# Kernel optimization log

Measured on AMD Instinct MI355X. Metric: run time of the kernel, lower is better.

Reference implementation:

```python
import jax, jax.numpy as jnp
import numpy as np

B, S, D = 256, 70, 128
NUM_NODE = 40000
N_SAMPLE = 12
ALPHA = 0.2  # leaky-relu slope


def setup_inputs() -> dict:
    key = jax.random.key(0)
    ks = jax.random.split(key, 16)
    stdv = 1.0 / np.sqrt(D)
    u = lambda k, shp: jax.random.uniform(k, shp, jnp.float32, -stdv, stdv)
    inputs = jax.random.randint(ks[0], (B, S), 0, NUM_NODE)
    adj = jax.random.randint(ks[1], (B, S, S), 0, 5)
    mask_item = jnp.ones((B, S), jnp.int32)
    item = jax.random.randint(ks[2], (B, S), 0, NUM_NODE)
    input_times = jax.random.uniform(ks[3], (B, S), jnp.float32)
    adj_all = jax.random.randint(ks[4], (NUM_NODE, N_SAMPLE), 0, NUM_NODE)
    num_w = jax.random.uniform(ks[5], (NUM_NODE, N_SAMPLE), jnp.float32)
    embedding = u(ks[6], (NUM_NODE, D))
    a0, a1, a2, a3 = (u(ks[7 + i], (D,)) for i in range(4))
    gw1 = u(ks[11], (D + 1, D))
    gw2 = u(ks[12], (D, 1))
    gw3 = u(ks[13], (2 * D, D))
    gbias = u(ks[14], (D,))
    return dict(inputs=inputs, adj=adj, mask_item=mask_item, item=item,
                input_times=input_times, adj_all=adj_all, num_w=num_w,
                embedding=embedding, a0=a0, a1=a1, a2=a2, a3=a3,
                gw1=gw1, gw2=gw2, gw3=gw3, gbias=gbias)


def reference(inputs, adj, mask_item, item, input_times, adj_all, num_w,
              embedding, a0, a1, a2, a3, gw1, gw2, gw3, gbias):
    # ---- local aggregator (4-relation GAT over session graph) ----
    h = embedding[inputs]                              # [B,S,D]
    a_in = h[:, :, None, :] * h[:, None, :, :]         # [B,S,S,D] pairwise products
    att = lambda a: jax.nn.leaky_relu(jnp.einsum('bijd,d->bij', a_in, a), ALPHA)
    e0, e1, e2, e3 = att(a0), att(a1), att(a2), att(a3)
    neg = jnp.full_like(e0, -9e15)
    alpha = jnp.where(adj == 1, e0, neg)
    alpha = jnp.where(adj == 2, e1, alpha)
    alpha = jnp.where(adj == 3, e2, alpha)
    alpha = jnp.where(adj == 4, e3, alpha)
    alpha = jax.nn.softmax(alpha, axis=-1)
    h_local = jnp.einsum('bij,bjd->bid', alpha, h)     # [B,S,D]

    # ---- global aggregator: 1-hop neighbor sampling + session-gated attention ----
    flat = inputs.reshape(-1)
    neigh = adj_all[flat].reshape(B, S, N_SAMPLE)      # sampled neighbor ids
    nw = num_w[flat].reshape(B, S, N_SAMPLE)           # neighbor co-occurrence weights
    nv = embedding[neigh]                              # [B,S,K,D]

    maskf = mask_item.astype(jnp.float32)[..., None]   # [B,S,1]
    item_emb = embedding[item] * maskf
    sess = jnp.sum(item_emb, axis=1) / jnp.sum(maskf, axis=1)   # [B,D] mean session emb
    extra = sess[:, None, None, :]                     # broadcast to [B,S,K,D]

    feat = jnp.concatenate([extra * nv, nw[..., None]], axis=-1)  # [B,S,K,D+1]
    al = jax.nn.leaky_relu(feat @ gw1, 0.2)            # [B,S,K,D]
    al = jax.nn.softmax((al @ gw2)[..., 0], axis=-1)[..., None]   # [B,S,K,1]
    nagg = jnp.sum(al * nv, axis=-2)                   # [B,S,D]

    out = jnp.concatenate([h, nagg], axis=-1) @ gw3 + gbias
    h_global = jax.nn.relu(out)                        # [B,S,D]
    # dropout_local/global = 0 (eval mode): identity
    return h_local, h_global
```

## Files before the change

kernel.cpp:

```cpp
#include <hip/hip_runtime.h>
#include <hip/hip_bf16.h>

#define B_ 256
#define S_ 70
#define D_ 128
#define NSAMP 12
#define HGLOB (B_ * S_ * D_)
#define IBLK 14
#define HTS 136
#define NPOS 10
#define NR2 (NPOS * NSAMP)
#define NRP 128

typedef float  f32x4 __attribute__((ext_vector_type(4)));
typedef short  s16x8 __attribute__((ext_vector_type(8)));

__device__ __forceinline__ unsigned short f2bf(float x) {
    union { float f; unsigned u; } v; v.f = x;
    return (unsigned short)((v.u + 0x7FFF + ((v.u >> 16) & 1)) >> 16);
}
__device__ __forceinline__ float bf2f(unsigned short u) {
    union { unsigned u; float f; } v; v.u = ((unsigned)u) << 16;
    return v.f;
}

__global__ __launch_bounds__(128) void sess_kernel(const int* __restrict__ item,
                                                   const int* __restrict__ mask,
                                                   const float* __restrict__ emb,
                                                   float* __restrict__ sess) {
    int b = blockIdx.x;
    int d = threadIdx.x;
    float acc = 0.f, msum = 0.f;
    for (int s = 0; s < S_; ++s) {
        int node = item[b * S_ + s];
        float m = (float)mask[b * S_ + s];
        acc += m * emb[(long)node * D_ + d];
        msum += m;
    }
    sess[b * D_ + d] = acc / msum;
}

__global__ __launch_bounds__(256) void pack_weights(const float* __restrict__ gw1,
                                                    const float* __restrict__ gw3,
                                                    unsigned short* __restrict__ gw1T,
                                                    unsigned short* __restrict__ gw3T) {
    int idx = blockIdx.x * 256 + threadIdx.x;
    if (idx < 128 * 128) {
        int c = idx >> 7, r = idx & 127;
        gw1T[idx] = f2bf(gw1[r * 128 + c]);
    }
    if (idx < 128 * 256) {
        int c = idx >> 8, r = idx & 255;
        gw3T[idx] = f2bf(gw3[r * 128 + c]);
    }
}

__global__ __launch_bounds__(256) void local_kernel(const int* __restrict__ inputs,
                                                    const int* __restrict__ adj,
                                                    const float* __restrict__ emb,
                                                    const float* __restrict__ a0p,
                                                    const float* __restrict__ a1p,
                                                    const float* __restrict__ a2p,
                                                    const float* __restrict__ a3p,
                                                    float* __restrict__ out) {
    __shared__ __align__(16) unsigned short hl[72 * 128];
    __shared__ __align__(16) unsigned short HT[128 * HTS];
    __shared__ __align__(16) float          El[16 * 84];
    __shared__ __align__(16) unsigned short al[16 * 104];
    __shared__ int ids[S_];

    const int b  = blockIdx.x;
    const int i0 = blockIdx.y * IBLK;
    const int tid  = threadIdx.x;
    const int lane = tid & 63, wave = tid >> 6;
    const int l15  = lane & 15, l4 = lane >> 4;

    const s16x8 zero8 = {0, 0, 0, 0, 0, 0, 0, 0};

    if (tid < S_) ids[tid] = inputs[b * S_ + tid];
    for (int c = tid; c < (128 * HTS) / 8; c += 256) ((s16x8*)HT)[c] = zero8;
    if (tid < 32) ((s16x8*)hl)[70 * 16 + tid] = zero8;
    __syncthreads();

    #pragma unroll
    for (int it = 0; it < 5; ++it) {
        int idx = it * 256 + tid;
        if (idx < S_ * 16) {
            int s = idx >> 4, c8 = idx & 15;
            const float4* ev = (const float4*)(emb + (long)ids[s] * D_ + c8 * 8);
            float4 e0 = ev[0], e1 = ev[1];
            s16x8 p;
            p[0] = (short)f2bf(e0.x); p[1] = (short)f2bf(e0.y);
            p[2] = (short)f2bf(e0.z); p[3] = (short)f2bf(e0.w);
            p[4] = (short)f2bf(e1.x); p[5] = (short)f2bf(e1.y);
            p[6] = (short)f2bf(e1.z); p[7] = (short)f2bf(e1.w);
            ((s16x8*)hl)[s * 16 + (c8 ^ (s & 7))] = p;
            #pragma unroll
            for (int e = 0; e < 8; ++e) {
                int d = c8 * 8 + e;
                HT[d * HTS + s] = (unsigned short)p[e];
            }
        }
    }
    __syncthreads();

    s16x8 af_all[4][4];
    {
        const float* aptr[4] = {a0p, a1p, a2p, a3p};
        int hrow = i0 + l15;
        #pragma unroll
        for (int ks = 0; ks < 4; ++ks) {
            s16x8 hf = ((s16x8*)hl)[hrow * 16 + ((ks * 4 + l4) ^ (hrow & 7))];
            #pragma unroll
            for (int r = 0; r < 4; ++r) {
                const float* ar = aptr[r];
                float4 alo = *(const float4*)(ar + ks * 32 + l4 * 8);
                float4 ahi = *(const float4*)(ar + ks * 32 + l4 * 8 + 4);
                s16x8 o;
                o[0] = (short)f2bf(bf2f((unsigned short)hf[0]) * alo.x);
                o[1] = (short)f2bf(bf2f((unsigned short)hf[1]) * alo.y);
                o[2] = (short)f2bf(bf2f((unsigned short)hf[2]) * alo.z);
                o[3] = (short)f2bf(bf2f((unsigned short)hf[3]) * alo.w);
                o[4] = (short)f2bf(bf2f((unsigned short)hf[4]) * ahi.x);
                o[5] = (short)f2bf(bf2f((unsigned short)hf[5]) * ahi.y);
                o[6] = (short)f2bf(bf2f((unsigned short)hf[6]) * ahi.z);
                o[7] = (short)f2bf(bf2f((unsigned short)hf[7]) * ahi.w);
                af_all[r][ks] = o;
            }
        }
    }

    for (int n = wave; n < 5; n += 4) {
        s16x8 bfr[4];
        int jr = n * 16 + l15;
        int jrc = jr < 72 ? jr : 71;
        #pragma unroll
        for (int ks = 0; ks < 4; ++ks)
            bfr[ks] = ((s16x8*)hl)[jrc * 16 + ((ks * 4 + l4) ^ (jrc & 7))];

        f32x4 ac0 = {0.f,0.f,0.f,0.f}, ac1 = {0.f,0.f,0.f,0.f};
        f32x4 ac2 = {0.f,0.f,0.f,0.f}, ac3 = {0.f,0.f,0.f,0.f};
        #pragma unroll
        for (int ks = 0; ks < 4; ++ks) {
            ac0 = __builtin_amdgcn_mfma_f32_16x16x32_bf16(af_all[0][ks], bfr[ks], ac0, 0, 0, 0);
            ac1 = __builtin_amdgcn_mfma_f32_16x16x32_bf16(af_all[1][ks], bfr[ks], ac1, 0, 0, 0);
            ac2 = __builtin_amdgcn_mfma_f32_16x16x32_bf16(af_all[2][ks], bfr[ks], ac2, 0, 0, 0);
            ac3 = __builtin_amdgcn_mfma_f32_16x16x32_bf16(af_all[3][ks], bfr[ks], ac3, 0, 0, 0);
        }

        #pragma unroll
        for (int reg = 0; reg < 4; ++reg) {
            int il = l4 * 4 + reg;
            int i  = i0 + il;
            int j  = n * 16 + l15;
            float v;
            if (j < S_) {
                int ic = i < S_ ? i : S_ - 1;
                int a  = adj[((long)b * S_ + ic) * S_ + j];
                float raw = (a == 1) ? ac0[reg] : (a == 2) ? ac1[reg]
                          : (a == 3) ? ac2[reg] : (a == 4) ? ac3[reg] : 0.f;
                v = (a >= 1 && a <= 4) ? (raw > 0.f ? raw : 0.2f * raw) : -9e15f;
            } else {
                v = -INFINITY;
            }
            El[il * 84 + j] = v;
        }
    }
    __syncthreads();

    {
        int g = tid >> 4, li = tid & 15;
        float mx = -INFINITY;
        for (int j = li; j < S_; j += 16) mx = fmaxf(mx, El[g * 84 + j]);
        #pragma unroll
        for (int o = 1; o < 16; o <<= 1) mx = fmaxf(mx, __shfl_xor(mx, o));
        float sm = 0.f;
        for (int j = li; j < S_; j += 16) {
            float ex = __expf(El[g * 84 + j] - mx);
            El[g * 84 + j] = ex;
            sm += ex;
        }
        #pragma unroll
        for (int o = 1; o < 16; o <<= 1) sm += __shfl_xor(sm, o);
        float inv = 1.f / sm;
        for (int j = li; j < 104; j += 16)
            al[g * 104 + j] = (j < S_) ? f2bf(El[g * 84 + j] * inv) : (unsigned short)0;
    }
    __syncthreads();

    for (int n = wave; n < 8; n += 4) {
        f32x4 acc = {0.f, 0.f, 0.f, 0.f};
        int d = n * 16 + l15;
        #pragma unroll
        for (int ks = 0; ks < 3; ++ks) {
            s16x8 afp = *(const s16x8*)(al + l15 * 104 + ks * 32 + l4 * 8);
            s16x8 bfp = *(const s16x8*)(HT + d * HTS + ks * 32 + l4 * 8);
            acc = __builtin_amdgcn_mfma_f32_16x16x32_bf16(afp, bfp, acc, 0, 0, 0);
        }
        #pragma unroll
        for (int reg = 0; reg < 4; ++reg) {
            int il = l4 * 4 + reg;
            if (il < IBLK)
                out[((long)b * S_ + (i0 + il)) * D_ + d] = acc[reg];
        }
    }
}

__global__ __launch_bounds__(256, 3) void global_kernel(
        const int* __restrict__ inputs, const int* __restrict__ adj_all,
        const float* __restrict__ num_w, const float* __restrict__ emb,
        const float* __restrict__ sess,
        const unsigned short* __restrict__ gw1T, const float* __restrict__ gw1,
        const float* __restrict__ gw2,
        const unsigned short* __restrict__ gw3T, const float* __restrict__ gbias,
        float* __restrict__ out) {
    __shared__ __align__(16) unsigned short nv[NRP * 128];
    __shared__ __align__(16) unsigned short cat[16 * 256];
    __shared__ int   neigh[NR2];
    __shared__ float nw[NR2];
    __shared__ float spart[NRP][4];
    __shared__ float score[NR2];
    __shared__ float wsm[NR2];

    const int tid  = threadIdx.x;
    const int lane = tid & 63, wave = tid >> 6;
    const int l15  = lane & 15, l4 = lane >> 4;
    const int b    = blockIdx.x;
    const int i0   = blockIdx.y * NPOS;
    const int bs0  = b * S_ + i0;

    const s16x8 zero8 = {0, 0, 0, 0, 0, 0, 0, 0};

    if (tid < NR2) {
        int p = tid / NSAMP;
        int k = tid - p * NSAMP;
        int node = inputs[bs0 + p];
        neigh[tid] = adj_all[node * NSAMP + k];
        nw[tid]    = num_w[node * NSAMP + k];
    }
    if (tid < 128) ((s16x8*)nv)[NR2 * 16 + tid] = zero8;
    __syncthreads();

    #pragma unroll
    for (int it = 0; it < 8; ++it) {
        int idx = it * 256 + tid;
        if (idx < NR2 * 16) {
            int row = idx >> 4, c8 = idx & 15;
            const float4* ev = (const float4*)(emb + (long)neigh[row] * D_ + c8 * 8);
            float4 e0 = ev[0], e1 = ev[1];
            s16x8 p;
            p[0] = (short)f2bf(e0.x); p[1] = (short)f2bf(e0.y);
            p[2] = (short)f2bf(e0.z); p[3] = (short)f2bf(e0.w);
            p[4] = (short)f2bf(e1.x); p[5] = (short)f2bf(e1.y);
            p[6] = (short)f2bf(e1.z); p[7] = (short)f2bf(e1.w);
            ((s16x8*)nv)[row * 16 + (c8 ^ (row & 7))] = p;
        }
    }
    __syncthreads();

    s16x8 bfp[2][4];
    #pragma unroll
    for (int n = 0; n < 2; ++n) {
        int c = (wave * 2 + n) * 16 + l15;
        #pragma unroll
        for (int ks = 0; ks < 4; ++ks) {
            s16x8 g = *(const s16x8*)(gw1T + c * 128 + ks * 32 + l4 * 8);
            float4 slo = *(const float4*)(sess + b * D_ + ks * 32 + l4 * 8);
            float4 shi = *(const float4*)(sess + b * D_ + ks * 32 + l4 * 8 + 4);
            s16x8 o;
            o[0] = (short)f2bf(bf2f((unsigned short)g[0]) * slo.x);
            o[1] = (short)f2bf(bf2f((unsigned short)g[1]) * slo.y);
            o[2] = (short)f2bf(bf2f((unsigned short)g[2]) * slo.z);
            o[3] = (short)f2bf(bf2f((unsigned short)g[3]) * slo.w);
            o[4] = (short)f2bf(bf2f((unsigned short)g[4]) * shi.x);
            o[5] = (short)f2bf(bf2f((unsigned short)g[5]) * shi.y);
            o[6] = (short)f2bf(bf2f((unsigned short)g[6]) * shi.z);
            o[7] = (short)f2bf(bf2f((unsigned short)g[7]) * shi.w);
            bfp[n][ks] = o;
        }
    }
    float g128a = gw1[128 * 128 + wave * 32 + l15];
    float g128b = gw1[128 * 128 + wave * 32 + 16 + l15];
    float gw2a  = gw2[wave * 32 + l15];
    float gw2b  = gw2[wave * 32 + 16 + l15];

    for (int m = 0; m < NRP / 16; ++m) {
        int arow = m * 16 + l15;
        s16x8 af[4];
        #pragma unroll
        for (int ks = 0; ks < 4; ++ks)
            af[ks] = ((s16x8*)nv)[arow * 16 + ((ks * 4 + l4) ^ (arow & 7))];

        f32x4 acc0 = {0.f, 0.f, 0.f, 0.f}, acc1 = {0.f, 0.f, 0.f, 0.f};
        #pragma unroll
        for (int ks = 0; ks < 4; ++ks) {
            acc0 = __builtin_amdgcn_mfma_f32_16x16x32_bf16(af[ks], bfp[0][ks], acc0, 0, 0, 0);
            acc1 = __builtin_amdgcn_mfma_f32_16x16x32_bf16(af[ks], bfp[1][ks], acc1, 0, 0, 0);
        }

        float sp[4];
        #pragma unroll
        for (int reg = 0; reg < 4; ++reg) {
            int r = m * 16 + l4 * 4 + reg;
            float nwv = (r < NR2) ? nw[r] : 0.f;
            float al0 = acc0[reg] + nwv * g128a;
            float al1 = acc1[reg] + nwv * g128b;
            al0 = al0 > 0.f ? al0 : 0.2f * al0;
            al1 = al1 > 0.f ? al1 : 0.2f * al1;
            sp[reg] = al0 * gw2a + al1 * gw2b;
        }
        #pragma unroll
        for (int off = 1; off < 16; off <<= 1) {
            #pragma unroll
            for (int reg = 0; reg < 4; ++reg) sp[reg] += __shfl_xor(sp[reg], off);
        }
        if (l15 == 0) {
            int rb = m * 16 + l4 * 4;
            #pragma unroll
            for (int reg = 0; reg < 4; ++reg) spart[rb + reg][wave] = sp[reg];
        }
    }
    __syncthreads();

    if (tid < NR2)
        score[tid] = spart[tid][0] + spart[tid][1] + spart[tid][2] + spart[tid][3];
    __syncthreads();

    if (tid < NPOS) {
        float mx = -1e30f;
        #pragma unroll
        for (int k = 0; k < NSAMP; ++k) mx = fmaxf(mx, score[tid * NSAMP + k]);
        float ex[NSAMP]; float ss = 0.f;
        #pragma unroll
        for (int k = 0; k < NSAMP; ++k) { ex[k] = __expf(score[tid * NSAMP + k] - mx); ss += ex[k]; }
        float inv = 1.f / ss;
        #pragma unroll
        for (int k = 0; k < NSAMP; ++k) wsm[tid * NSAMP + k] = ex[k] * inv;
    }
    __syncthreads();

    {
        int p  = tid >> 4;
        int c8 = tid & 15;
        if (p < NPOS) {
            float a0v[4] = {0.f,0.f,0.f,0.f}, a1v[4] = {0.f,0.f,0.f,0.f};
            #pragma unroll
            for (int k = 0; k < NSAMP; ++k) {
                int row = p * NSAMP + k;
                float w = wsm[row];
                s16x8 nvv = ((s16x8*)nv)[row * 16 + (c8 ^ (row & 7))];
                a0v[0] += w * bf2f((unsigned short)nvv[0]);
                a0v[1] += w * bf2f((unsigned short)nvv[1]);
                a0v[2] += w * bf2f((unsigned short)nvv[2]);
                a0v[3] += w * bf2f((unsigned short)nvv[3]);
                a1v[0] += w * bf2f((unsigned short)nvv[4]);
                a1v[1] += w * bf2f((unsigned short)nvv[5]);
                a1v[2] += w * bf2f((unsigned short)nvv[6]);
                a1v[3] += w * bf2f((unsigned short)nvv[7]);
            }
            int node = inputs[bs0 + p];
            const float4* hv = (const float4*)(emb + (long)node * D_ + c8 * 8);
            float4 h0 = hv[0], h1 = hv[1];
            s16x8 ph, pa;
            ph[0]=(short)f2bf(h0.x); ph[1]=(short)f2bf(h0.y); ph[2]=(short)f2bf(h0.z); ph[3]=(short)f2bf(h0.w);
            ph[4]=(short)f2bf(h1.x); ph[5]=(short)f2bf(h1.y); ph[6]=(short)f2bf(h1.z); ph[7]=(short)f2bf(h1.w);
            pa[0]=(short)f2bf(a0v[0]); pa[1]=(short)f2bf(a0v[1]); pa[2]=(short)f2bf(a0v[2]); pa[3]=(short)f2bf(a0v[3]);
            pa[4]=(short)f2bf(a1v[0]); pa[5]=(short)f2bf(a1v[1]); pa[6]=(short)f2bf(a1v[2]); pa[7]=(short)f2bf(a1v[3]);
            ((s16x8*)cat)[p * 32 + ( c8       ^ (p & 7))] = ph;
            ((s16x8*)cat)[p * 32 + ((16 + c8) ^ (p & 7))] = pa;
        } else {
            ((s16x8*)cat)[p * 32 + ( c8       ^ (p & 7))] = zero8;
            ((s16x8*)cat)[p * 32 + ((16 + c8) ^ (p & 7))] = zero8;
        }
    }
    __syncthreads();

    {
        f32x4 acc0 = {0.f,0.f,0.f,0.f}, acc1 = {0.f,0.f,0.f,0.f};
        int arow = l15;
        int cc = wave * 32 + l15;
        #pragma unroll
        for (int ks = 0; ks < 8; ++ks) {
            s16x8 a  = ((s16x8*)cat)[arow * 32 + ((ks * 4 + l4) ^ (arow & 7))];
            s16x8 b0 = *(const s16x8*)(gw3T +  cc       * 256 + ks * 32 + l4 * 8);
            s16x8 b1 = *(const s16x8*)(gw3T + (cc + 16) * 256 + ks * 32 + l4 * 8);
            acc0 = __builtin_amdgcn_mfma_f32_16x16x32_bf16(a, b0, acc0, 0, 0, 0);
            acc1 = __builtin_amdgcn_mfma_f32_16x16x32_bf16(a, b1, acc1, 0, 0, 0);
        }
        float gb0 = gbias[wave * 32 + l15];
        float gb1 = gbias[wave * 32 + 16 + l15];
        #pragma unroll
        for (int reg = 0; reg < 4; ++reg) {
            int il = l4 * 4 + reg;
            if (il < NPOS) {
                long bs = bs0 + il;
                float o0 = acc0[reg] + gb0;
                float o1 = acc1[reg] + gb1;
                out[(long)HGLOB + bs * D_ + wave * 32 + l15]      = o0 > 0.f ? o0 : 0.f;
                out[(long)HGLOB + bs * D_ + wave * 32 + 16 + l15] = o1 > 0.f ? o1 : 0.f;
            }
        }
    }
}

extern "C" void kernel_launch(void* const* d_in, const int* in_sizes, int n_in,
                              void* d_out, int out_size, void* d_ws, size_t ws_size,
                              hipStream_t stream) {
    const int*   inputs  = (const int*)  d_in[0];
    const int*   adj     = (const int*)  d_in[1];
    const int*   mask    = (const int*)  d_in[2];
    const int*   item    = (const int*)  d_in[3];
    const int*   adj_all = (const int*)  d_in[5];
    const float* num_w   = (const float*)d_in[6];
    const float* emb     = (const float*)d_in[7];
    const float* a0      = (const float*)d_in[8];
    const float* a1      = (const float*)d_in[9];
    const float* a2      = (const float*)d_in[10];
    const float* a3      = (const float*)d_in[11];
    const float* gw1     = (const float*)d_in[12];
    const float* gw2     = (const float*)d_in[13];
    const float* gw3     = (const float*)d_in[14];
    const float* gbias   = (const float*)d_in[15];
    float* out = (float*)d_out;

    float*          sess = (float*)d_ws;
    unsigned short* gw1T = (unsigned short*)((char*)d_ws + 131072);
    unsigned short* gw3T = gw1T + 128 * 128;

    sess_kernel<<<B_, D_, 0, stream>>>(item, mask, emb, sess);
    pack_weights<<<128, 256, 0, stream>>>(gw1, gw3, gw1T, gw3T);
    local_kernel<<<dim3(B_, 5), 256, 0, stream>>>(inputs, adj, emb, a0, a1, a2, a3, out);
    global_kernel<<<dim3(B_, 7), 256, 0, stream>>>(inputs, adj_all, num_w, emb, sess,
                                                   gw1T, gw1, gw2, gw3T, gbias, out);
}
```

Before: 97.67 us.

## Gather neighbor embeddings directly from global memory instead of staging in LDS

Removes the 32KB shared-memory staging buffer for neighbor embeddings. The MFMA A-fragments are loaded and converted to bf16 straight from global memory, and the weighted neighbor sum re-reads the fp32 rows from global. This cuts LDS use and one barrier to raise occupancy, and the launch-bounds occupancy hint is dropped. In exchange every wave reloads the same rows and each row is fetched twice, relying on L2/L1 caching, and the global loads now sit directly on the MFMA path.

Result: slower. 129.2 us (+32.3%).

```diff
diff --git a/kernel.cpp b/kernel.cpp
--- a/kernel.cpp
+++ b/kernel.cpp
@@ -206,7 +206,7 @@
     }
 }
 
-__global__ __launch_bounds__(256, 3) void global_kernel(
+__global__ __launch_bounds__(256) void global_kernel(
         const int* __restrict__ inputs, const int* __restrict__ adj_all,
         const float* __restrict__ num_w, const float* __restrict__ emb,
         const float* __restrict__ sess,
@@ -214,7 +214,6 @@
         const float* __restrict__ gw2,
         const unsigned short* __restrict__ gw3T, const float* __restrict__ gbias,
         float* __restrict__ out) {
-    __shared__ __align__(16) unsigned short nv[NRP * 128];
     __shared__ __align__(16) unsigned short cat[16 * 256];
     __shared__ int   neigh[NR2];
     __shared__ float nw[NR2];
@@ -237,24 +236,6 @@
         int node = inputs[bs0 + p];
         neigh[tid] = adj_all[node * NSAMP + k];
         nw[tid]    = num_w[node * NSAMP + k];
-    }
-    if (tid < 128) ((s16x8*)nv)[NR2 * 16 + tid] = zero8;
-    __syncthreads();
-
-    #pragma unroll
-    for (int it = 0; it < 8; ++it) {
-        int idx = it * 256 + tid;
-        if (idx < NR2 * 16) {
-            int row = idx >> 4, c8 = idx & 15;
-            const float4* ev = (const float4*)(emb + (long)neigh[row] * D_ + c8 * 8);
-            float4 e0 = ev[0], e1 = ev[1];
-            s16x8 p;
-            p[0] = (short)f2bf(e0.x); p[1] = (short)f2bf(e0.y);
-            p[2] = (short)f2bf(e0.z); p[3] = (short)f2bf(e0.w);
-            p[4] = (short)f2bf(e1.x); p[5] = (short)f2bf(e1.y);
-            p[6] = (short)f2bf(e1.z); p[7] = (short)f2bf(e1.w);
-            ((s16x8*)nv)[row * 16 + (c8 ^ (row & 7))] = p;
-        }
     }
     __syncthreads();
 
@@ -284,12 +265,32 @@
     float gw2a  = gw2[wave * 32 + l15];
     float gw2b  = gw2[wave * 32 + 16 + l15];
 
+    long nbase[8];
+    #pragma unroll
+    for (int m = 0; m < 8; ++m) {
+        int row = m * 16 + l15;
+        nbase[m] = (row < NR2) ? (long)neigh[row] * D_ : -1;
+    }
+
     for (int m = 0; m < NRP / 16; ++m) {
-        int arow = m * 16 + l15;
         s16x8 af[4];
-        #pragma unroll
-        for (int ks = 0; ks < 4; ++ks)
-            af[ks] = ((s16x8*)nv)[arow * 16 + ((ks * 4 + l4) ^ (arow & 7))];
+        if (nbase[m] >= 0) {
+            const float* rp = emb + nbase[m] + l4 * 8;
+            #pragma unroll
+            for (int ks = 0; ks < 4; ++ks) {
+                float4 e0 = *(const float4*)(rp + ks * 32);
+                float4 e1 = *(const float4*)(rp + ks * 32 + 4);
+                s16x8 p;
+                p[0] = (short)f2bf(e0.x); p[1] = (short)f2bf(e0.y);
+                p[2] = (short)f2bf(e0.z); p[3] = (short)f2bf(e0.w);
+                p[4] = (short)f2bf(e1.x); p[5] = (short)f2bf(e1.y);
+                p[6] = (short)f2bf(e1.z); p[7] = (short)f2bf(e1.w);
+                af[ks] = p;
+            }
+        } else {
+            #pragma unroll
+            for (int ks = 0; ks < 4; ++ks) af[ks] = zero8;
+        }
 
         f32x4 acc0 = {0.f, 0.f, 0.f, 0.f}, acc1 = {0.f, 0.f, 0.f, 0.f};
         #pragma unroll
@@ -348,15 +349,10 @@
             for (int k = 0; k < NSAMP; ++k) {
                 int row = p * NSAMP + k;
                 float w = wsm[row];
-                s16x8 nvv = ((s16x8*)nv)[row * 16 + (c8 ^ (row & 7))];
-                a0v[0] += w * bf2f((unsigned short)nvv[0]);
-                a0v[1] += w * bf2f((unsigned short)nvv[1]);
-                a0v[2] += w * bf2f((unsigned short)nvv[2]);
-                a0v[3] += w * bf2f((unsigned short)nvv[3]);
-                a1v[0] += w * bf2f((unsigned short)nvv[4]);
-                a1v[1] += w * bf2f((unsigned short)nvv[5]);
-                a1v[2] += w * bf2f((unsigned short)nvv[6]);
-                a1v[3] += w * bf2f((unsigned short)nvv[7]);
+                const float4* ev = (const float4*)(emb + (long)neigh[row] * D_ + c8 * 8);
+                float4 e0 = ev[0], e1 = ev[1];
+                a0v[0] += w * e0.x; a0v[1] += w * e0.y; a0v[2] += w * e0.z; a0v[3] += w * e0.w;
+                a1v[0] += w * e1.x; a1v[1] += w * e1.y; a1v[2] += w * e1.z; a1v[3] += w * e1.w;
             }
             int node = inputs[bs0 + p];
             const float4* hv = (const float4*)(emb + (long)node * D_ + c8 * 8);
```

## Fuse local and global aggregators into one kernel and parallelize session mean

Applied to the files above, without the earlier changes.

Merges the local and global kernels into a single launch of B*12 blocks that branch on block index, with a shared-memory union sized for the larger global layout. The separate transposed HT tile is removed from the local path, shrinking its LDS use. The session-mean kernel now splits the sequence over four thread groups and reduces in shared memory. The aim is to cut launch overhead and the tail between the two kernels, and to raise occupancy. The cost is divergent block types with uneven work and the loss of the global kernel's launch_bounds occupancy hint.

Result: faster. 83.98 us (-14.0%).

```diff
diff --git a/kernel.cpp b/kernel.cpp
--- a/kernel.cpp
+++ b/kernel.cpp
@@ -7,7 +7,6 @@
 #define NSAMP 12
 #define HGLOB (B_ * S_ * D_)
 #define IBLK 14
-#define HTS 136
 #define NPOS 10
 #define NR2 (NPOS * NSAMP)
 #define NRP 128
@@ -24,20 +23,29 @@
     return v.f;
 }
 
-__global__ __launch_bounds__(128) void sess_kernel(const int* __restrict__ item,
+__global__ __launch_bounds__(512) void sess_kernel(const int* __restrict__ item,
                                                    const int* __restrict__ mask,
                                                    const float* __restrict__ emb,
                                                    float* __restrict__ sess) {
+    __shared__ float pacc[4][D_];
+    __shared__ float pm[4];
     int b = blockIdx.x;
-    int d = threadIdx.x;
+    int d = threadIdx.x & 127, q = threadIdx.x >> 7;
     float acc = 0.f, msum = 0.f;
-    for (int s = 0; s < S_; ++s) {
+    for (int s = q; s < S_; s += 4) {
         int node = item[b * S_ + s];
         float m = (float)mask[b * S_ + s];
         acc += m * emb[(long)node * D_ + d];
         msum += m;
     }
-    sess[b * D_ + d] = acc / msum;
+    pacc[q][d] = acc;
+    if (d == 0) pm[q] = msum;
+    __syncthreads();
+    if (q == 0) {
+        float a = pacc[0][d] + pacc[1][d] + pacc[2][d] + pacc[3][d];
+        float m = pm[0] + pm[1] + pm[2] + pm[3];
+        sess[b * D_ + d] = a / m;
+    }
 }
 
 __global__ __launch_bounds__(256) void pack_weights(const float* __restrict__ gw1,
@@ -55,349 +63,349 @@
     }
 }
 
-__global__ __launch_bounds__(256) void local_kernel(const int* __restrict__ inputs,
-                                                    const int* __restrict__ adj,
-                                                    const float* __restrict__ emb,
-                                                    const float* __restrict__ a0p,
-                                                    const float* __restrict__ a1p,
-                                                    const float* __restrict__ a2p,
-                                                    const float* __restrict__ a3p,
-                                                    float* __restrict__ out) {
-    __shared__ __align__(16) unsigned short hl[72 * 128];
-    __shared__ __align__(16) unsigned short HT[128 * HTS];
-    __shared__ __align__(16) float          El[16 * 84];
-    __shared__ __align__(16) unsigned short al[16 * 104];
-    __shared__ int ids[S_];
-
-    const int b  = blockIdx.x;
-    const int i0 = blockIdx.y * IBLK;
-    const int tid  = threadIdx.x;
-    const int lane = tid & 63, wave = tid >> 6;
-    const int l15  = lane & 15, l4 = lane >> 4;
-
-    const s16x8 zero8 = {0, 0, 0, 0, 0, 0, 0, 0};
-
-    if (tid < S_) ids[tid] = inputs[b * S_ + tid];
-    for (int c = tid; c < (128 * HTS) / 8; c += 256) ((s16x8*)HT)[c] = zero8;
-    if (tid < 32) ((s16x8*)hl)[70 * 16 + tid] = zero8;
-    __syncthreads();
-
-    #pragma unroll
-    for (int it = 0; it < 5; ++it) {
-        int idx = it * 256 + tid;
-        if (idx < S_ * 16) {
-            int s = idx >> 4, c8 = idx & 15;
-            const float4* ev = (const float4*)(emb + (long)ids[s] * D_ + c8 * 8);
-            float4 e0 = ev[0], e1 = ev[1];
-            s16x8 p;
-            p[0] = (short)f2bf(e0.x); p[1] = (short)f2bf(e0.y);
-            p[2] = (short)f2bf(e0.z); p[3] = (short)f2bf(e0.w);
-            p[4] = (short)f2bf(e1.x); p[5] = (short)f2bf(e1.y);
-            p[6] = (short)f2bf(e1.z); p[7] = (short)f2bf(e1.w);
-            ((s16x8*)hl)[s * 16 + (c8 ^ (s & 7))] = p;
-            #pragma unroll
-            for (int e = 0; e < 8; ++e) {
-                int d = c8 * 8 + e;
-                HT[d * HTS + s] = (unsigned short)p[e];
-            }
-        }
-    }
-    __syncthreads();
-
-    s16x8 af_all[4][4];
-    {
-        const float* aptr[4] = {a0p, a1p, a2p, a3p};
-        int hrow = i0 + l15;
-        #pragma unroll
-        for (int ks = 0; ks < 4; ++ks) {
-            s16x8 hf = ((s16x8*)hl)[hrow * 16 + ((ks * 4 + l4) ^ (hrow & 7))];
-            #pragma unroll
-            for (int r = 0; r < 4; ++r) {
-                const float* ar = aptr[r];
-                float4 alo = *(const float4*)(ar + ks * 32 + l4 * 8);
-                float4 ahi = *(const float4*)(ar + ks * 32 + l4 * 8 + 4);
-                s16x8 o;
-                o[0] = (short)f2bf(bf2f((unsigned short)hf[0]) * alo.x);
-                o[1] = (short)f2bf(bf2f((unsigned short)hf[1]) * alo.y);
-                o[2] = (short)f2bf(bf2f((unsigned short)hf[2]) * alo.z);
-                o[3] = (short)f2bf(bf2f((unsigned short)hf[3]) * alo.w);
-                o[4] = (short)f2bf(bf2f((unsigned short)hf[4]) * ahi.x);
-                o[5] = (short)f2bf(bf2f((unsigned short)hf[5]) * ahi.y);
-                o[6] = (short)f2bf(bf2f((unsigned short)hf[6]) * ahi.z);
-                o[7] = (short)f2bf(bf2f((unsigned short)hf[7]) * ahi.w);
-                af_all[r][ks] = o;
-            }
-        }
-    }
-
-    for (int n = wave; n < 5; n += 4) {
-        s16x8 bfr[4];
-        int jr = n * 16 + l15;
-        int jrc = jr < 72 ? jr : 71;
-        #pragma unroll
-        for (int ks = 0; ks < 4; ++ks)
-            bfr[ks] = ((s16x8*)hl)[jrc * 16 + ((ks * 4 + l4) ^ (jrc & 7))];
-
-        f32x4 ac0 = {0.f,0.f,0.f,0.f}, ac1 = {0.f,0.f,0.f,0.f};
-        f32x4 ac2 = {0.f,0.f,0.f,0.f}, ac3 = {0.f,0.f,0.f,0.f};
-        #pragma unroll
-        for (int ks = 0; ks < 4; ++ks) {
-            ac0 = __builtin_amdgcn_mfma_f32_16x16x32_bf16(af_all[0][ks], bfr[ks], ac0, 0, 0, 0);
-            ac1 = __builtin_amdgcn_mfma_f32_16x16x32_bf16(af_all[1][ks], bfr[ks], ac1, 0, 0, 0);
-            ac2 = __builtin_amdgcn_mfma_f32_16x16x32_bf16(af_all[2][ks], bfr[ks], ac2, 0, 0, 0);
-            ac3 = __builtin_amdgcn_mfma_f32_16x16x32_bf16(af_all[3][ks], bfr[ks], ac3, 0, 0, 0);
-        }
-
-        #pragma unroll
-        for (int reg = 0; reg < 4; ++reg) {
-            int il = l4 * 4 + reg;
-            int i  = i0 + il;
-            int j  = n * 16 + l15;
-            float v;
-            if (j < S_) {
-                int ic = i < S_ ? i : S_ - 1;
-                int a  = adj[((long)b * S_ + ic) * S_ + j];
-                float raw = (a == 1) ? ac0[reg] : (a == 2) ? ac1[reg]
-                          : (a == 3) ? ac2[reg] : (a == 4) ? ac3[reg] : 0.f;
-                v = (a >= 1 && a <= 4) ? (raw > 0.f ? raw : 0.2f * raw) : -9e15f;
-            } else {
-                v = -INFINITY;
-            }
-            El[il * 84 + j] = v;
-        }
-    }
-    __syncthreads();
-
-    {
-        int g = tid >> 4, li = tid & 15;
-        float mx = -INFINITY;
-        for (int j = li; j < S_; j += 16) mx = fmaxf(mx, El[g * 84 + j]);
-        #pragma unroll
-        for (int o = 1; o < 16; o <<= 1) mx = fmaxf(mx, __shfl_xor(mx, o));
-        float sm = 0.f;
-        for (int j = li; j < S_; j += 16) {
-            float ex = __expf(El[g * 84 + j] - mx);
-            El[g * 84 + j] = ex;
-            sm += ex;
-        }
-        #pragma unroll
-        for (int o = 1; o < 16; o <<= 1) sm += __shfl_xor(sm, o);
-        float inv = 1.f / sm;
-        for (int j = li; j < 104; j += 16)
-            al[g * 104 + j] = (j < S_) ? f2bf(El[g * 84 + j] * inv) : (unsigned short)0;
-    }
-    __syncthreads();
-
-    for (int n = wave; n < 8; n += 4) {
-        f32x4 acc = {0.f, 0.f, 0.f, 0.f};
-        int d = n * 16 + l15;
-        #pragma unroll
-        for (int ks = 0; ks < 3; ++ks) {
-            s16x8 afp = *(const s16x8*)(al + l15 * 104 + ks * 32 + l4 * 8);
-            s16x8 bfp = *(const s16x8*)(HT + d * HTS + ks * 32 + l4 * 8);
-            acc = __builtin_amdgcn_mfma_f32_16x16x32_bf16(afp, bfp, acc, 0, 0, 0);
-        }
-        #pragma unroll
-        for (int reg = 0; reg < 4; ++reg) {
-            int il = l4 * 4 + reg;
-            if (il < IBLK)
-                out[((long)b * S_ + (i0 + il)) * D_ + d] = acc[reg];
-        }
-    }
-}
-
-__global__ __launch_bounds__(256, 3) void global_kernel(
-        const int* __restrict__ inputs, const int* __restrict__ adj_all,
-        const float* __restrict__ num_w, const float* __restrict__ emb,
-        const float* __restrict__ sess,
+struct LocalSM {
+    unsigned short hl[72 * 128];
+    float          El[16 * 84];
+    unsigned short al[16 * 104];
+    int            ids[72];
+};
+struct GlobalSM {
+    unsigned short nv[NRP * 128];
+    unsigned short cat[16 * 256];
+    float          spart[NRP][4];
+    int            neigh[NR2];
+    float          nw[NR2];
+    float          score[NR2];
+    float          wsm[NR2];
+};
+
+__global__ __launch_bounds__(256) void fused_kernel(
+        const int* __restrict__ inputs, const int* __restrict__ adj,
+        const int* __restrict__ adj_all, const float* __restrict__ num_w,
+        const float* __restrict__ emb, const float* __restrict__ sess,
+        const float* __restrict__ a0p, const float* __restrict__ a1p,
+        const float* __restrict__ a2p, const float* __restrict__ a3p,
         const unsigned short* __restrict__ gw1T, const float* __restrict__ gw1,
         const float* __restrict__ gw2,
         const unsigned short* __restrict__ gw3T, const float* __restrict__ gbias,
         float* __restrict__ out) {
-    __shared__ __align__(16) unsigned short nv[NRP * 128];
-    __shared__ __align__(16) unsigned short cat[16 * 256];
-    __shared__ int   neigh[NR2];
-    __shared__ float nw[NR2];
-    __shared__ float spart[NRP][4];
-    __shared__ float score[NR2];
-    __shared__ float wsm[NR2];
-
+    __shared__ __align__(16) char smem[sizeof(GlobalSM)];
+
+    const int L = blockIdx.x;
+    const int b = L / 12;
+    const int r = L - b * 12;
     const int tid  = threadIdx.x;
     const int lane = tid & 63, wave = tid >> 6;
     const int l15  = lane & 15, l4 = lane >> 4;
-    const int b    = blockIdx.x;
-    const int i0   = blockIdx.y * NPOS;
-    const int bs0  = b * S_ + i0;
-
     const s16x8 zero8 = {0, 0, 0, 0, 0, 0, 0, 0};
 
-    if (tid < NR2) {
-        int p = tid / NSAMP;
-        int k = tid - p * NSAMP;
-        int node = inputs[bs0 + p];
-        neigh[tid] = adj_all[node * NSAMP + k];
-        nw[tid]    = num_w[node * NSAMP + k];
-    }
-    if (tid < 128) ((s16x8*)nv)[NR2 * 16 + tid] = zero8;
-    __syncthreads();
-
-    #pragma unroll
-    for (int it = 0; it < 8; ++it) {
-        int idx = it * 256 + tid;
-        if (idx < NR2 * 16) {
-            int row = idx >> 4, c8 = idx & 15;
-            const float4* ev = (const float4*)(emb + (long)neigh[row] * D_ + c8 * 8);
-            float4 e0 = ev[0], e1 = ev[1];
-            s16x8 p;
-            p[0] = (short)f2bf(e0.x); p[1] = (short)f2bf(e0.y);
-            p[2] = (short)f2bf(e0.z); p[3] = (short)f2bf(e0.w);
-            p[4] = (short)f2bf(e1.x); p[5] = (short)f2bf(e1.y);
-            p[6] = (short)f2bf(e1.z); p[7] = (short)f2bf(e1.w);
-            ((s16x8*)nv)[row * 16 + (c8 ^ (row & 7))] = p;
-        }
-    }
-    __syncthreads();
-
-    s16x8 bfp[2][4];
-    #pragma unroll
-    for (int n = 0; n < 2; ++n) {
-        int c = (wave * 2 + n) * 16 + l15;
+    if (r < 5) {
+        LocalSM* P = (LocalSM*)smem;
+        const int i0 = r * IBLK;
+
+        if (tid < S_) P->ids[tid] = inputs[b * S_ + tid];
+        if (tid < 32) ((s16x8*)P->hl)[70 * 16 + tid] = zero8;
+        __syncthreads();
+
         #pragma unroll
-        for (int ks = 0; ks < 4; ++ks) {
-            s16x8 g = *(const s16x8*)(gw1T + c * 128 + ks * 32 + l4 * 8);
-            float4 slo = *(const float4*)(sess + b * D_ + ks * 32 + l4 * 8);
-            float4 shi = *(const float4*)(sess + b * D_ + ks * 32 + l4 * 8 + 4);
-            s16x8 o;
-            o[0] = (short)f2bf(bf2f((unsigned short)g[0]) * slo.x);
-            o[1] = (short)f2bf(bf2f((unsigned short)g[1]) * slo.y);
-            o[2] = (short)f2bf(bf2f((unsigned short)g[2]) * slo.z);
-            o[3] = (short)f2bf(bf2f((unsigned short)g[3]) * slo.w);
-            o[4] = (short)f2bf(bf2f((unsigned short)g[4]) * shi.x);
-            o[5] = (short)f2bf(bf2f((unsigned short)g[5]) * shi.y);
-            o[6] = (short)f2bf(bf2f((unsigned short)g[6]) * shi.z);
-            o[7] = (short)f2bf(bf2f((unsigned short)g[7]) * shi.w);
-            bfp[n][ks] = o;
-        }
-    }
-    float g128a = gw1[128 * 128 + wave * 32 + l15];
-    float g128b = gw1[128 * 128 + wave * 32 + 16 + l15];
-    float gw2a  = gw2[wave * 32 + l15];
-    float gw2b  = gw2[wave * 32 + 16 + l15];
-
-    for (int m = 0; m < NRP / 16; ++m) {
-        int arow = m * 16 + l15;
-        s16x8 af[4];
+        for (int it = 0; it < 5; ++it) {
+            int idx = it * 256 + tid;
+            if (idx < S_ * 16) {
+                int s = idx >> 4, c8 = idx & 15;
+                const float4* ev = (const float4*)(emb + (long)P->ids[s] * D_ + c8 * 8);
+                float4 e0 = ev[0], e1 = ev[1];
+                s16x8 p;
+                p[0] = (short)f2bf(e0.x); p[1] = (short)f2bf(e0.y);
+                p[2] = (short)f2bf(e0.z); p[3] = (short)f2bf(e0.w);
+                p[4] = (short)f2bf(e1.x); p[5] = (short)f2bf(e1.y);
+                p[6] = (short)f2bf(e1.z); p[7] = (short)f2bf(e1.w);
+                ((s16x8*)P->hl)[s * 16 + (c8 ^ (s & 7))] = p;
+            }
+        }
+        __syncthreads();
+
+        s16x8 af_all[4][4];
+        {
+            const float* aptr[4] = {a0p, a1p, a2p, a3p};
+            int hrow = i0 + l15;
+            #pragma unroll
+            for (int ks = 0; ks < 4; ++ks) {
+                s16x8 hf = ((s16x8*)P->hl)[hrow * 16 + ((ks * 4 + l4) ^ (hrow & 7))];
+                #pragma unroll
+                for (int rr = 0; rr < 4; ++rr) {
+                    const float* ar = aptr[rr];
+                    float4 alo = *(const float4*)(ar + ks * 32 + l4 * 8);
+                    float4 ahi = *(const float4*)(ar + ks * 32 + l4 * 8 + 4);
+                    s16x8 o;
+                    o[0] = (short)f2bf(bf2f((unsigned short)hf[0]) * alo.x);
+                    o[1] = (short)f2bf(bf2f((unsigned short)hf[1]) * alo.y);
+                    o[2] = (short)f2bf(bf2f((unsigned short)hf[2]) * alo.z);
+                    o[3] = (short)f2bf(bf2f((unsigned short)hf[3]) * alo.w);
+                    o[4] = (short)f2bf(bf2f((unsigned short)hf[4]) * ahi.x);
+                    o[5] = (short)f2bf(bf2f((unsigned short)hf[5]) * ahi.y);
+                    o[6] = (short)f2bf(bf2f((unsigned short)hf[6]) * ahi.z);
+                    o[7] = (short)f2bf(bf2f((unsigned short)hf[7]) * ahi.w);
+                    af_all[rr][ks] = o;
+                }
+            }
+        }
+
+        for (int n = wave; n < 5; n += 4) {
+            s16x8 bfr[4];
+            int jr = n * 16 + l15;
+            int jrc = jr < 72 ? jr : 71;
+            #pragma unroll
+            for (int ks = 0; ks < 4; ++ks)
+                bfr[ks] = ((s16x8*)P->hl)[jrc * 16 + ((ks * 4 + l4) ^ (jrc & 7))];
+
+            f32x4 ac0 = {0.f,0.f,0.f,0.f}, ac1 = {0.f,0.f,0.f,0.f};
+            f32x4 ac2 = {0.f,0.f,0.f,0.f}, ac3 = {0.f,0.f,0.f,0.f};
+            #pragma unroll
+            for (int ks = 0; ks < 4; ++ks) {
+                ac0 = __builtin_amdgcn_mfma_f32_16x16x32_bf16(af_all[0][ks], bfr[ks], ac0, 0, 0, 0);
+                ac1 = __builtin_amdgcn_mfma_f32_16x16x32_bf16(af_all[1][ks], bfr[ks], ac1, 0, 0, 0);
+                ac2 = __builtin_amdgcn_mfma_f32_16x16x32_bf16(af_all[2][ks], bfr[ks], ac2, 0, 0, 0);
+                ac3 = __builtin_amdgcn_mfma_f32_16x16x32_bf16(af_all[3][ks], bfr[ks], ac3, 0, 0, 0);
+            }
+
+            #pragma unroll
+            for (int reg = 0; reg < 4; ++reg) {
+                int il = l4 * 4 + reg;
+                int i  = i0 + il;
+                int j  = n * 16 + l15;
+                float v;
+                if (j < S_) {
+                    int ic = i < S_ ? i : S_ - 1;
+                    int a  = adj[((long)b * S_ + ic) * S_ + j];
+                    float raw = (a == 1) ? ac0[reg] : (a == 2) ? ac1[reg]
+                              : (a == 3) ? ac2[reg] : (a == 4) ? ac3[reg] : 0.f;
+                    v = (a >= 1 && a <= 4) ? (raw > 0.f ? raw : 0.2f * raw) : -9e15f;
+                } else {
+                    v = -INFINITY;
+                }
+                P->El[il * 84 + j] = v;
+            }
+        }
+        __syncthreads();
+
+        {
+            int g = tid >> 4, li = tid & 15;
+            float mx = -INFINITY;
+            for (int j = li; j < S_; j += 16) mx = fmaxf(mx, P->El[g * 84 + j]);
+            #pragma unroll
+            for (int o = 1; o < 16; o <<= 1) mx = fmaxf(mx, __shfl_xor(mx, o));
+            float sm = 0.f;
+            for (int j = li; j < S_; j += 16) {
+                float ex = __expf(P->El[g * 84 + j] - mx);
+                P->El[g * 84 + j] = ex;
+                sm += ex;
+            }
+            #pragma unroll
+            for (int o = 1; o < 16; o <<= 1) sm += __shfl_xor(sm, o);
+            float inv = 1.f / sm;
+            for (int j = li; j < 104; j += 16)
+                P->al[g * 104 + j] = (j < S_) ? f2bf(P->El[g * 84 + j] * inv) : (unsigned short)0;
+        }
+        __syncthreads();
+
+        for (int n = wave; n < 8; n += 4) {
+            f32x4 acc = {0.f, 0.f, 0.f, 0.f};
+            int d = n * 16 + l15;
+            int dchunk = d >> 3, de = d & 7;
+            #pragma unroll
+            for (int ks = 0; ks < 3; ++ks) {
+                s16x8 afp = *(const s16x8*)(P->al + l15 * 104 + ks * 32 + l4 * 8);
+                int jb = ks * 32 + l4 * 8;
+                s16x8 bfp;
+                #pragma unroll
+                for (int e = 0; e < 8; ++e) {
+                    int j = jb + e;
+                    bfp[e] = (j < 72)
+                        ? (short)P->hl[j * 128 + ((dchunk ^ (j & 7)) << 3) + de]
+                        : (short)0;
+                }
+                acc = __builtin_amdgcn_mfma_f32_16x16x32_bf16(afp, bfp, acc, 0, 0, 0);
+            }
+            #pragma unroll
+            for (int reg = 0; reg < 4; ++reg) {
+                int il = l4 * 4 + reg;
+                if (il < IBLK)
+                    out[((long)b * S_ + (i0 + il)) * D_ + d] = acc[reg];
+            }
+        }
+    } else {
+        GlobalSM* P = (GlobalSM*)smem;
+        const int i0  = (r - 5) * NPOS;
+        const int bs0 = b * S_ + i0;
+
+        if (tid < NR2) {
+            int p = tid / NSAMP;
+            int k = tid - p * NSAMP;
+            int node = inputs[bs0 + p];
+            P->neigh[tid] = adj_all[node * NSAMP + k];
+            P->nw[tid]    = num_w[node * NSAMP + k];
+        }
+        if (tid < 128) ((s16x8*)P->nv)[NR2 * 16 + tid] = zero8;
+        __syncthreads();
+
         #pragma unroll
-        for (int ks = 0; ks < 4; ++ks)
-            af[ks] = ((s16x8*)nv)[arow * 16 + ((ks * 4 + l4) ^ (arow & 7))];
-
-        f32x4 acc0 = {0.f, 0.f, 0.f, 0.f}, acc1 = {0.f, 0.f, 0.f, 0.f};
+        for (int it = 0; it < 8; ++it) {
+            int idx = it * 256 + tid;
+            if (idx < NR2 * 16) {
+                int row = idx >> 4, c8 = idx & 15;
+                const float4* ev = (const float4*)(emb + (long)P->neigh[row] * D_ + c8 * 8);
+                float4 e0 = ev[0], e1 = ev[1];
+                s16x8 p;
+                p[0] = (short)f2bf(e0.x); p[1] = (short)f2bf(e0.y);
+                p[2] = (short)f2bf(e0.z); p[3] = (short)f2bf(e0.w);
+                p[4] = (short)f2bf(e1.x); p[5] = (short)f2bf(e1.y);
+                p[6] = (short)f2bf(e1.z); p[7] = (short)f2bf(e1.w);
+                ((s16x8*)P->nv)[row * 16 + (c8 ^ (row & 7))] = p;
+            }
+        }
+        __syncthreads();
+
+        s16x8 bfp[2][4];
         #pragma unroll
-        for (int ks = 0; ks < 4; ++ks) {
-            acc0 = __builtin_amdgcn_mfma_f32_16x16x32_bf16(af[ks], bfp[0][ks], acc0, 0, 0, 0);
-            acc1 = __builtin_amdgcn_mfma_f32_16x16x32_bf16(af[ks], bfp[1][ks], acc1, 0, 0, 0);
-        }
-
-        float sp[4];
-        #pragma unroll
-        for (int reg = 0; reg < 4; ++reg) {
-            int r = m * 16 + l4 * 4 + reg;
-            float nwv = (r < NR2) ? nw[r] : 0.f;
-            float al0 = acc0[reg] + nwv * g128a;
-            float al1 = acc1[reg] + nwv * g128b;
-            al0 = al0 > 0.f ? al0 : 0.2f * al0;
-            al1 = al1 > 0.f ? al1 : 0.2f * al1;
-            sp[reg] = al0 * gw2a + al1 * gw2b;
-        }
-        #pragma unroll
-        for (int off = 1; off < 16; off <<= 1) {
-            #pragma unroll
-            for (int reg = 0; reg < 4; ++reg) sp[reg] += __shfl_xor(sp[reg], off);
-        }
-        if (l15 == 0) {
-            int rb = m * 16 + l4 * 4;
-            #pragma unroll
-            for (int reg = 0; reg < 4; ++reg) spart[rb + reg][wave] = sp[reg];
-        }
-    }
-    __syncthreads();
-
-    if (tid < NR2)
-        score[tid] = spart[tid][0] + spart[tid][1] + spart[tid][2] + spart[tid][3];
-    __syncthreads();
-
-    if (tid < NPOS) {
-        float mx = -1e30f;
-        #pragma unroll
-        for (int k = 0; k < NSAMP; ++k) mx = fmaxf(mx, score[tid * NSAMP + k]);
-        float ex[NSAMP]; float ss = 0.f;
-        #pragma unroll
-        for (int k = 0; k < NSAMP; ++k) { ex[k] = __expf(score[tid * NSAMP + k] - mx); ss += ex[k]; }
-        float inv = 1.f / ss;
-        #pragma unroll
-        for (int k = 0; k < NSAMP; ++k) wsm[tid * NSAMP + k] = ex[k] * inv;
-    }
-    __syncthreads();
-
-    {
-        int p  = tid >> 4;
-        int c8 = tid & 15;
-        if (p < NPOS) {
-            float a0v[4] = {0.f,0.f,0.f,0.f}, a1v[4] = {0.f,0.f,0.f,0.f};
-            #pragma unroll
-            for (int k = 0; k < NSAMP; ++k) {
-                int row = p * NSAMP + k;
-                float w = wsm[row];
-                s16x8 nvv = ((s16x8*)nv)[row * 16 + (c8 ^ (row & 7))];
-                a0v[0] += w * bf2f((unsigned short)nvv[0]);
-                a0v[1] += w * bf2f((unsigned short)nvv[1]);
-                a0v[2] += w * bf2f((unsigned short)nvv[2]);
-                a0v[3] += w * bf2f((unsigned short)nvv[3]);
-                a1v[0] += w * bf2f((unsigned short)nvv[4]);
-                a1v[1] += w * bf2f((unsigned short)nvv[5]);
-                a1v[2] += w * bf2f((unsigned short)nvv[6]);
-                a1v[3] += w * bf2f((unsigned short)nvv[7]);
-            }
-            int node = inputs[bs0 + p];
-            const float4* hv = (const float4*)(emb + (long)node * D_ + c8 * 8);
-            float4 h0 = hv[0], h1 = hv[1];
-            s16x8 ph, pa;
-            ph[0]=(short)f2bf(h0.x); ph[1]=(short)f2bf(h0.y); ph[2]=(short)f2bf(h0.z); ph[3]=(short)f2bf(h0.w);
-            ph[4]=(short)f2bf(h1.x); ph[5]=(short)f2bf(h1.y); ph[6]=(short)f2bf(h1.z); ph[7]=(short)f2bf(h1.w);
-            pa[0]=(short)f2bf(a0v[0]); pa[1]=(short)f2bf(a0v[1]); pa[2]=(short)f2bf(a0v[2]); pa[3]=(short)f2bf(a0v[3]);
-            pa[4]=(short)f2bf(a1v[0]); pa[5]=(short)f2bf(a1v[1]); pa[6]=(short)f2bf(a1v[2]); pa[7]=(short)f2bf(a1v[3]);
-            ((s16x8*)cat)[p * 32 + ( c8       ^ (p & 7))] = ph;
-            ((s16x8*)cat)[p * 32 + ((16 + c8) ^ (p & 7))] = pa;
-        } else {
-            ((s16x8*)cat)[p * 32 + ( c8       ^ (p & 7))] = zero8;
-            ((s16x8*)cat)[p * 32 + ((16 + c8) ^ (p & 7))] = zero8;
-        }
-    }
-    __syncthreads();
-
-    {
-        f32x4 acc0 = {0.f,0.f,0.f,0.f}, acc1 = {0.f,0.f,0.f,0.f};
-        int arow = l15;
-        int cc = wave * 32 + l15;
-        #pragma unroll
-        for (int ks = 0; ks < 8; ++ks) {
-            s16x8 a  = ((s16x8*)cat)[arow * 32 + ((ks * 4 + l4) ^ (arow & 7))];
-            s16x8 b0 = *(const s16x8*)(gw3T +  cc       * 256 + ks * 32 + l4 * 8);
-            s16x8 b1 = *(const s16x8*)(gw3T + (cc + 16) * 256 + ks * 32 + l4 * 8);
-            acc0 = __builtin_amdgcn_mfma_f32_16x16x32_bf16(a, b0, acc0, 0, 0, 0);
-            acc1 = __builtin_amdgcn_mfma_f32_16x16x32_bf16(a, b1, acc1, 0, 0, 0);
-        }
-        float gb0 = gbias[wave * 32 + l15];
-        float gb1 = gbias[wave * 32 + 16 + l15];
-        #pragma unroll
-        for (int reg = 0; reg < 4; ++reg) {
-            int il = l4 * 4 + reg;
-            if (il < NPOS) {
-                long bs = bs0 + il;
-                float o0 = acc0[reg] + gb0;
-                float o1 = acc1[reg] + gb1;
-                out[(long)HGLOB + bs * D_ + wave * 32 + l15]      = o0 > 0.f ? o0 : 0.f;
-                out[(long)HGLOB + bs * D_ + wave * 32 + 16 + l15] = o1 > 0.f ? o1 : 0.f;
+        for (int n = 0; n < 2; ++n) {
+            int c = (wave * 2 + n) * 16 + l15;
+            #pragma unroll
+            for (int ks = 0; ks < 4; ++ks) {
+                s16x8 g = *(const s16x8*)(gw1T + c * 128 + ks * 32 + l4 * 8);
+                float4 slo = *(const float4*)(sess + b * D_ + ks * 32 + l4 * 8);
+                float4 shi = *(const float4*)(sess + b * D_ + ks * 32 + l4 * 8 + 4);
+                s16x8 o;
+                o[0] = (short)f2bf(bf2f((unsigned short)g[0]) * slo.x);
+                o[1] = (short)f2bf(bf2f((unsigned short)g[1]) * slo.y);
+                o[2] = (short)f2bf(bf2f((unsigned short)g[2]) * slo.z);
+                o[3] = (short)f2bf(bf2f((unsigned short)g[3]) * slo.w);
+                o[4] = (short)f2bf(bf2f((unsigned short)g[4]) * shi.x);
+                o[5] = (short)f2bf(bf2f((unsigned short)g[5]) * shi.y);
+                o[6] = (short)f2bf(bf2f((unsigned short)g[6]) * shi.z);
+                o[7] = (short)f2bf(bf2f((unsigned short)g[7]) * shi.w);
+                bfp[n][ks] = o;
+            }
+        }
+        float g128a = gw1[128 * 128 + wave * 32 + l15];
+        float g128b = gw1[128 * 128 + wave * 32 + 16 + l15];
+        float gw2a  = gw2[wave * 32 + l15];
+        float gw2b  = gw2[wave * 32 + 16 + l15];
+
+        for (int m = 0; m < NRP / 16; ++m) {
+            int arow = m * 16 + l15;
+            s16x8 af[4];
+            #pragma unroll
+            for (int ks = 0; ks < 4; ++ks)
+                af[ks] = ((s16x8*)P->nv)[arow * 16 + ((ks * 4 + l4) ^ (arow & 7))];
+
+            f32x4 acc0 = {0.f, 0.f, 0.f, 0.f}, acc1 = {0.f, 0.f, 0.f, 0.f};
+            #pragma unroll
+            for (int ks = 0; ks < 4; ++ks) {
+                acc0 = __builtin_amdgcn_mfma_f32_16x16x32_bf16(af[ks], bfp[0][ks], acc0, 0, 0, 0);
+                acc1 = __builtin_amdgcn_mfma_f32_16x16x32_bf16(af[ks], bfp[1][ks], acc1, 0, 0, 0);
+            }
+
+            float sp[4];
+            #pragma unroll
+            for (int reg = 0; reg < 4; ++reg) {
+                int rr = m * 16 + l4 * 4 + reg;
+                float nwv = (rr < NR2) ? P->nw[rr] : 0.f;
+                float al0 = acc0[reg] + nwv * g128a;
+                float al1 = acc1[reg] + nwv * g128b;
+                al0 = al0 > 0.f ? al0 : 0.2f * al0;
+                al1 = al1 > 0.f ? al1 : 0.2f * al1;
+                sp[reg] = al0 * gw2a + al1 * gw2b;
+            }
+            #pragma unroll
+            for (int off = 1; off < 16; off <<= 1) {
+                #pragma unroll
+                for (int reg = 0; reg < 4; ++reg) sp[reg] += __shfl_xor(sp[reg], off);
+            }
+            if (l15 == 0) {
+                int rb = m * 16 + l4 * 4;
+                #pragma unroll
+                for (int reg = 0; reg < 4; ++reg) P->spart[rb + reg][wave] = sp[reg];
+            }
+        }
+        __syncthreads();
+
+        if (tid < NR2)
+            P->score[tid] = P->spart[tid][0] + P->spart[tid][1] + P->spart[tid][2] + P->spart[tid][3];
+        __syncthreads();
+
+        if (tid < NPOS) {
+            float mx = -1e30f;
+            #pragma unroll
+            for (int k = 0; k < NSAMP; ++k) mx = fmaxf(mx, P->score[tid * NSAMP + k]);
+            float ex[NSAMP]; float ss = 0.f;
+            #pragma unroll
+            for (int k = 0; k < NSAMP; ++k) { ex[k] = __expf(P->score[tid * NSAMP + k] - mx); ss += ex[k]; }
+            float inv = 1.f / ss;
+            #pragma unroll
+            for (int k = 0; k < NSAMP; ++k) P->wsm[tid * NSAMP + k] = ex[k] * inv;
+        }
+        __syncthreads();
+
+        {
+            int p  = tid >> 4;
+            int c8 = tid & 15;
+            if (p < NPOS) {
+                float a0v[4] = {0.f,0.f,0.f,0.f}, a1v[4] = {0.f,0.f,0.f,0.f};
+                #pragma unroll
+                for (int k = 0; k < NSAMP; ++k) {
+                    int row = p * NSAMP + k;
+                    float w = P->wsm[row];
+                    s16x8 nvv = ((s16x8*)P->nv)[row * 16 + (c8 ^ (row & 7))];
+                    a0v[0] += w * bf2f((unsigned short)nvv[0]);
+                    a0v[1] += w * bf2f((unsigned short)nvv[1]);
+                    a0v[2] += w * bf2f((unsigned short)nvv[2]);
+                    a0v[3] += w * bf2f((unsigned short)nvv[3]);
+                    a1v[0] += w * bf2f((unsigned short)nvv[4]);
+                    a1v[1] += w * bf2f((unsigned short)nvv[5]);
+                    a1v[2] += w * bf2f((unsigned short)nvv[6]);
+                    a1v[3] += w * bf2f((unsigned short)nvv[7]);
+                }
+                int node = inputs[bs0 + p];
+                const float4* hv = (const float4*)(emb + (long)node * D_ + c8 * 8);
+                float4 h0 = hv[0], h1 = hv[1];
+                s16x8 ph, pa;
+                ph[0]=(short)f2bf(h0.x); ph[1]=(short)f2bf(h0.y); ph[2]=(short)f2bf(h0.z); ph[3]=(short)f2bf(h0.w);
+                ph[4]=(short)f2bf(h1.x); ph[5]=(short)f2bf(h1.y); ph[6]=(short)f2bf(h1.z); ph[7]=(short)f2bf(h1.w);
+                pa[0]=(short)f2bf(a0v[0]); pa[1]=(short)f2bf(a0v[1]); pa[2]=(short)f2bf(a0v[2]); pa[3]=(short)f2bf(a0v[3]);
+                pa[4]=(short)f2bf(a1v[0]); pa[5]=(short)f2bf(a1v[1]); pa[6]=(short)f2bf(a1v[2]); pa[7]=(short)f2bf(a1v[3]);
+                ((s16x8*)P->cat)[p * 32 + ( c8       ^ (p & 7))] = ph;
+                ((s16x8*)P->cat)[p * 32 + ((16 + c8) ^ (p & 7))] = pa;
+            } else {
+                ((s16x8*)P->cat)[p * 32 + ( c8       ^ (p & 7))] = zero8;
+                ((s16x8*)P->cat)[p * 32 + ((16 + c8) ^ (p & 7))] = zero8;
+            }
+        }
+        __syncthreads();
+
+        {
+            f32x4 acc0 = {0.f,0.f,0.f,0.f}, acc1 = {0.f,0.f,0.f,0.f};
+            int arow = l15;
+            int cc = wave * 32 + l15;
+            #pragma unroll
+            for (int ks = 0; ks < 8; ++ks) {
+                s16x8 a  = ((s16x8*)P->cat)[arow * 32 + ((ks * 4 + l4) ^ (arow & 7))];
+                s16x8 b0 = *(const s16x8*)(gw3T +  cc       * 256 + ks * 32 + l4 * 8);
+                s16x8 b1 = *(const s16x8*)(gw3T + (cc + 16) * 256 + ks * 32 + l4 * 8);
+                acc0 = __builtin_amdgcn_mfma_f32_16x16x32_bf16(a, b0, acc0, 0, 0, 0);
+                acc1 = __builtin_amdgcn_mfma_f32_16x16x32_bf16(a, b1, acc1, 0, 0, 0);
+            }
+            float gb0 = gbias[wave * 32 + l15];
+            float gb1 = gbias[wave * 32 + 16 + l15];
+            #pragma unroll
+            for (int reg = 0; reg < 4; ++reg) {
+                int il = l4 * 4 + reg;
+                if (il < NPOS) {
+                    long bs = bs0 + il;
+                    float o0 = acc0[reg] + gb0;
+                    float o1 = acc1[reg] + gb1;
+                    out[(long)HGLOB + bs * D_ + wave * 32 + l15]      = o0 > 0.f ? o0 : 0.f;
+                    out[(long)HGLOB + bs * D_ + wave * 32 + 16 + l15] = o1 > 0.f ? o1 : 0.f;
+                }
             }
         }
     }
@@ -427,9 +435,9 @@
     unsigned short* gw1T = (unsigned short*)((char*)d_ws + 131072);
     unsigned short* gw3T = gw1T + 128 * 128;
 
-    sess_kernel<<<B_, D_, 0, stream>>>(item, mask, emb, sess);
+    sess_kernel<<<B_, 512, 0, stream>>>(item, mask, emb, sess);
     pack_weights<<<128, 256, 0, stream>>>(gw1, gw3, gw1T, gw3T);
-    local_kernel<<<dim3(B_, 5), 256, 0, stream>>>(inputs, adj, emb, a0, a1, a2, a3, out);
-    global_kernel<<<dim3(B_, 7), 256, 0, stream>>>(inputs, adj_all, num_w, emb, sess,
-                                                   gw1T, gw1, gw2, gw3T, gbias, out);
-}
+    fused_kernel<<<B_ * 12, 256, 0, stream>>>(inputs, adj, adj_all, num_w, emb, sess,
+                                              a0, a1, a2, a3,
+                                              gw1T, gw1, gw2, gw3T, gbias, out);
+}
```
